# Kernel optimization log

Measured on AMD Instinct MI355X. Metric: run time of the kernel, lower is better.

The kernel has to match this reference:

```python
import jax, jax.numpy as jnp
import numpy as np

N_NODES = 50000
N_EDGES = 800000
N_FEAT = 32
DIM_ENC = 64
HEADS = 8
DIM_MLP = 512
NUM_GRAPHS = 2000
NEG_SLOPE = 0.2


def gat_conv(x, edge_index, W, a_src, a_dst, bias, concat):
    """PyG-style GATConv: add self loops, per-head attention, segment softmax over
    incoming edges at the destination node, weighted scatter-sum aggregation."""
    N = x.shape[0]
    H, F = a_src.shape
    h = (x @ W).reshape(N, H, F)                      # [N, H, F]
    loop = jnp.arange(N, dtype=edge_index.dtype)
    src = jnp.concatenate([edge_index[0], loop])      # source j
    dst = jnp.concatenate([edge_index[1], loop])      # target i
    alpha_src = (h * a_src[None]).sum(-1)             # [N, H]
    alpha_dst = (h * a_dst[None]).sum(-1)             # [N, H]
    e = alpha_src[src] + alpha_dst[dst]               # [E', H]
    e = jnp.where(e > 0, e, NEG_SLOPE * e)            # leaky_relu
    # segment softmax over edges sharing the same destination node
    m = jax.ops.segment_max(e, dst, num_segments=N)
    ex = jnp.exp(e - m[dst])
    s = jax.ops.segment_sum(ex, dst, num_segments=N)
    alpha = ex / (s[dst] + 1e-16)                     # [E', H]
    msg = h[src] * alpha[..., None]                   # [E', H, F]
    out = jax.ops.segment_sum(msg, dst, num_segments=N)  # [N, H, F]
    out = out.reshape(N, H * F) if concat else out.mean(axis=1)
    return out + bias


def setup_inputs() -> dict:
    key = jax.random.key(0)
    ks = jax.random.split(key, 16)
    x = jax.random.normal(ks[0], (N_NODES, N_FEAT), dtype=jnp.float32)
    edge_index = jax.random.randint(ks[1], (2, N_EDGES), 0, N_NODES, dtype=jnp.int64)
    batch = jnp.sort(jax.random.randint(ks[2], (N_NODES,), 0, NUM_GRAPHS, dtype=jnp.int64))
    sc = lambda fi, fo: 1.0 / np.sqrt(fi)
    W1 = jax.random.normal(ks[3], (N_FEAT, HEADS * DIM_ENC), dtype=jnp.float32) * sc(N_FEAT, 0)
    a_src1 = jax.random.normal(ks[4], (HEADS, DIM_ENC), dtype=jnp.float32) * sc(DIM_ENC, 0)
    a_dst1 = jax.random.normal(ks[5], (HEADS, DIM_ENC), dtype=jnp.float32) * sc(DIM_ENC, 0)
    b1 = jnp.zeros((DIM_ENC,), dtype=jnp.float32)
    W2 = jax.random.normal(ks[6], (DIM_ENC, HEADS * DIM_ENC), dtype=jnp.float32) * sc(DIM_ENC, 0)
    a_src2 = jax.random.normal(ks[7], (HEADS, DIM_ENC), dtype=jnp.float32) * sc(DIM_ENC, 0)
    a_dst2 = jax.random.normal(ks[8], (HEADS, DIM_ENC), dtype=jnp.float32) * sc(DIM_ENC, 0)
    b2 = jnp.zeros((HEADS * DIM_ENC,), dtype=jnp.float32)
    fcW1 = jax.random.normal(ks[9], (HEADS * DIM_ENC, DIM_MLP), dtype=jnp.float32) * sc(HEADS * DIM_ENC, 0)
    fcb1 = jnp.zeros((DIM_MLP,), dtype=jnp.float32)
    fcW2 = jax.random.normal(ks[10], (DIM_MLP, DIM_MLP), dtype=jnp.float32) * sc(DIM_MLP, 0)
    fcb2 = jnp.zeros((DIM_MLP,), dtype=jnp.float32)
    fcW3 = jax.random.normal(ks[11], (DIM_MLP, 1), dtype=jnp.float32) * sc(DIM_MLP, 0)
    fcb3 = jnp.zeros((1,), dtype=jnp.float32)
    return dict(x=x, edge_index=edge_index, batch=batch,
                W1=W1, a_src1=a_src1, a_dst1=a_dst1, b1=b1,
                W2=W2, a_src2=a_src2, a_dst2=a_dst2, b2=b2,
                fcW1=fcW1, fcb1=fcb1, fcW2=fcW2, fcb2=fcb2, fcW3=fcW3, fcb3=fcb3)


def reference(x, edge_index, batch, W1, a_src1, a_dst1, b1, W2, a_src2, a_dst2, b2,
              fcW1, fcb1, fcW2, fcb2, fcW3, fcb3):
    h = gat_conv(x, edge_index, W1, a_src1, a_dst1, b1, concat=False)   # [N, dim_enc]
    h = gat_conv(h, edge_index, W2, a_src2, a_dst2, b2, concat=True)    # [N, 8*dim_enc]
    g = jax.ops.segment_sum(h, batch, num_segments=NUM_GRAPHS)          # [G, 8*dim_enc]
    g = jax.nn.relu(g @ fcW1 + fcb1)   # dropout is identity in eval / p=0
    g = jax.nn.relu(g @ fcW2 + fcb2)
    return g @ fcW3 + fcb3             # [G, 1]
```

## Files before the change

### kernel.cpp

```cpp
#include <hip/hip_runtime.h>
#include <hip/hip_bf16.h>

#define N_NODES   50000
#define N_EDGES   800000
#define NF        32
#define DE        64
#define NH        8
#define CT        512
#define DMLP      512
#define NG        2000
#define NEGS      0.2f


__device__ inline float4 fma4(float a, float4 v, float4 c) {
    c.x = fmaf(a, v.x, c.x); c.y = fmaf(a, v.y, c.y);
    c.z = fmaf(a, v.z, c.z); c.w = fmaf(a, v.w, c.w);
    return c;
}

__device__ inline float edge_w(float e) {
    e = e > 0.f ? e : NEGS * e;
    return __expf(e);
}


#define SB_A 1563
#define SB_I 196
#define SB_U 64
#define SB_G 196
#define SB_B 2

__global__ __launch_bounds__(256) void setup_k(
        const float* __restrict__ x, const float* __restrict__ W1,
        const float* __restrict__ as1, const float* __restrict__ ad1,
        const float* __restrict__ W2, const float* __restrict__ as2,
        const float* __restrict__ ad2, const int* __restrict__ batch,
        int* __restrict__ cnt, int* __restrict__ cur, int* __restrict__ total,
        float* __restrict__ U1, int* __restrict__ goff,
        float* __restrict__ B2s, float* __restrict__ B2d,
        float* __restrict__ as_, float* __restrict__ ad_) {
    int b = blockIdx.x;
    int tid = threadIdx.x;
    if (b < SB_A) {
        __shared__ float bs[256], bd[256];
        {
            int c = tid >> 3, hd = tid & 7;
            const float* wr = W1 + c * 512 + hd * 64;
            const float* p1 = as1 + hd * 64;
            const float* p2 = ad1 + hd * 64;
            float s1 = 0.f, s2 = 0.f;
            #pragma unroll 8
            for (int f = 0; f < 64; ++f) { float w = wr[f]; s1 += w * p1[f]; s2 += w * p2[f]; }
            bs[tid] = s1; bd[tid] = s2;
        }
        __syncthreads();
        int gid = b * 256 + tid;
        if (gid < N_NODES * NH) {
            int n = gid >> 3, hd = gid & 7;
            const float4* xp = (const float4*)(x + (size_t)n * NF);
            float s1 = 0.f, s2 = 0.f;
            #pragma unroll
            for (int qq = 0; qq < NF / 4; ++qq) {
                float4 v = xp[qq];
                int b0 = qq * 32 + hd;
                s1 += v.x * bs[b0] + v.y * bs[b0 + 8] + v.z * bs[b0 + 16] + v.w * bs[b0 + 24];
                s2 += v.x * bd[b0] + v.y * bd[b0 + 8] + v.z * bd[b0 + 16] + v.w * bd[b0 + 24];
            }
            as_[gid] = s1;
            ad_[gid] = s2;
        }
    } else if (b < SB_A + SB_I) {
        int i = (b - SB_A) * 256 + tid;
        if (i < N_NODES) { cnt[i] = 1; cur[i] = 0; }
        if (i == 0) total[0] = 0;
    } else if (b < SB_A + SB_I + SB_U) {
        int i = (b - SB_A - SB_I) * 256 + tid;
        int k = i >> 6, f = i & 63;
        int hd = k >> 5, c = k & 31;
        U1[i] = W1[c * 512 + hd * 64 + f] * 0.125f;
    } else if (b < SB_A + SB_I + SB_U + SB_G) {
        int i = (b - SB_A - SB_I - SB_U) * 256 + tid;
        if (i < N_NODES) {
            int bb = batch[i];
            if (i == 0) {
                for (int g = 0; g <= bb; ++g) goff[g] = 0;
            } else {
                int pb = batch[i - 1];
                for (int g = pb + 1; g <= bb; ++g) goff[g] = i;
            }
            if (i == N_NODES - 1) {
                for (int g = bb + 1; g <= NG; ++g) goff[g] = N_NODES;
            }
        }
    } else {
        int i = (b - SB_A - SB_I - SB_U - SB_G) * 256 + tid;
        int c = i >> 3, hd = i & 7;
        const float* wr = W2 + c * 512 + hd * 64;
        const float* p1 = as2 + hd * 64;
        const float* p2 = ad2 + hd * 64;
        float s1 = 0.f, s2 = 0.f;
        #pragma unroll 8
        for (int f = 0; f < 64; ++f) { float w = wr[f]; s1 += w * p1[f]; s2 += w * p2[f]; }
        B2s[i] = s1; B2d[i] = s2;
    }
}


__global__ void hist_k(const int* __restrict__ ei, int* __restrict__ cnt) {
    int e = blockIdx.x * 256 + threadIdx.x;
    if (e < N_EDGES) atomicAdd(&cnt[ei[N_EDGES + e]], 1);
}

__global__ void alloc_off_k(const int* __restrict__ cnt, int* __restrict__ off,
                            int* __restrict__ total) {
    int i = blockIdx.x * 256 + threadIdx.x;
    if (i < N_NODES) off[i] = atomicAdd(total, cnt[i]);
}

__global__ void scatter_k(const int* __restrict__ ei, const int* __restrict__ off,
                          int* __restrict__ cur, int* __restrict__ ssrc) {
    int e = blockIdx.x * 256 + threadIdx.x;
    if (e < N_EDGES) {
        int s = ei[e];
        int d = ei[N_EDGES + e];
        int p = off[d] + atomicAdd(&cur[d], 1);
        ssrc[p] = s;
    } else if (e < N_EDGES + N_NODES) {
        int i = e - N_EDGES;
        int p = off[i] + atomicAdd(&cur[i], 1);
        ssrc[p] = i;
    }
}


__global__ void alpha2_k(const float* __restrict__ hx, const float* __restrict__ Bs,
                         const float* __restrict__ Bd, float* __restrict__ as_,
                         float* __restrict__ ad_) {
    __shared__ float bs[512], bd[512];
    int tid = threadIdx.x;
    for (int i = tid; i < 512; i += 256) { bs[i] = Bs[i]; bd[i] = Bd[i]; }
    __syncthreads();
    int gid = blockIdx.x * 256 + tid;
    if (gid >= N_NODES * NH) return;
    int n = gid >> 3, hd = gid & 7;
    const float4* xp = (const float4*)(hx + (size_t)n * DE);
    float s1 = 0.f, s2 = 0.f;
    #pragma unroll
    for (int qq = 0; qq < DE / 4; ++qq) {
        float4 v = xp[qq];
        int b0 = qq * 32 + hd;
        s1 += v.x * bs[b0] + v.y * bs[b0 + 8] + v.z * bs[b0 + 16] + v.w * bs[b0 + 24];
        s2 += v.x * bd[b0] + v.y * bd[b0 + 8] + v.z * bd[b0 + 16] + v.w * bd[b0 + 24];
    }
    as_[gid] = s1;
    ad_[gid] = s2;
}


__global__ __launch_bounds__(256) void agg1_k(
        const float* __restrict__ x, const float* __restrict__ as_,
        const float* __restrict__ ad_, const int* __restrict__ ssrc,
        const int* __restrict__ off, const int* __restrict__ cnt,
        float* __restrict__ aggx1) {
    int wv = __builtin_amdgcn_readfirstlane(blockIdx.x * 4 + (threadIdx.x >> 6));
    if (wv >= N_NODES) return;
    int lane = threadIdx.x & 63;
    int hd = lane >> 3, q = lane & 7;
    int beg = off[wv], end = beg + cnt[wv];
    float adv = ad_[wv * NH + hd];

    float4 acc = {0.f, 0.f, 0.f, 0.f};
    float wsum = 0.f;
    int j = beg;
    for (; j + 8 <= end; j += 8) {
        int s[8]; float ev[8]; float4 v[8];
        #pragma unroll
        for (int u = 0; u < 8; ++u) s[u] = ssrc[j + u];
        #pragma unroll
        for (int u = 0; u < 8; ++u) ev[u] = as_[s[u] * NH + hd];
        #pragma unroll
        for (int u = 0; u < 8; ++u) v[u] = *(const float4*)(x + s[u] * NF + q * 4);
        #pragma unroll
        for (int u = 0; u < 8; ++u) {
            float w = edge_w(ev[u] + adv);
            wsum += w;
            acc = fma4(w, v[u], acc);
        }
    }
    for (; j < end; ++j) {
        int s0 = ssrc[j];
        float w0 = edge_w(as_[s0 * NH + hd] + adv);
        float4 v0 = *(const float4*)(x + s0 * NF + q * 4);
        wsum += w0;
        acc = fma4(w0, v0, acc);
    }
    float inv = 1.f / wsum;
    acc.x *= inv; acc.y *= inv; acc.z *= inv; acc.w *= inv;
    ((float4*)(aggx1 + (size_t)wv * 256))[lane] = acc;
}


template<int K, int N, bool RELU>
__global__ __launch_bounds__(256) void tgemm_k(
        const float* __restrict__ A, const float* __restrict__ W,
        const float* __restrict__ bias, float* __restrict__ Y, int nrows) {
    constexpr int KC = (K < 256) ? K : 256;
    __shared__ float As[KC][64];
    int t = threadIdx.x;
    int row0 = blockIdx.x * 64;
    int col0 = blockIdx.y * 64;
    int rr = t & 63;
    int kb = (t >> 6) * (KC / 4);
    int r0 = (t >> 4) * 4;
    int c0 = (t & 15) * 4;
    float acc[4][4];
    #pragma unroll
    for (int i = 0; i < 4; ++i)
        #pragma unroll
        for (int j = 0; j < 4; ++j) acc[i][j] = 0.f;

    for (int kc = 0; kc < K; kc += KC) {
        if (kc) __syncthreads();
        {
            int grow = row0 + rr;
            const float* ap = A + (size_t)grow * K + kc + kb;
            #pragma unroll
            for (int i = 0; i < KC / 4; i += 4) {
                float4 v = {0.f, 0.f, 0.f, 0.f};
                if (grow < nrows) v = *(const float4*)(ap + i);
                As[kb + i + 0][rr] = v.x;
                As[kb + i + 1][rr] = v.y;
                As[kb + i + 2][rr] = v.z;
                As[kb + i + 3][rr] = v.w;
            }
        }
        __syncthreads();
        const float* wp = W + (size_t)kc * N + col0 + c0;
        #pragma unroll 4
        for (int k = 0; k < KC; ++k) {
            float4 a = *(const float4*)&As[k][r0];
            float4 w = *(const float4*)(wp + (size_t)k * N);
            acc[0][0] = fmaf(a.x, w.x, acc[0][0]); acc[0][1] = fmaf(a.x, w.y, acc[0][1]);
            acc[0][2] = fmaf(a.x, w.z, acc[0][2]); acc[0][3] = fmaf(a.x, w.w, acc[0][3]);
            acc[1][0] = fmaf(a.y, w.x, acc[1][0]); acc[1][1] = fmaf(a.y, w.y, acc[1][1]);
            acc[1][2] = fmaf(a.y, w.z, acc[1][2]); acc[1][3] = fmaf(a.y, w.w, acc[1][3]);
            acc[2][0] = fmaf(a.z, w.x, acc[2][0]); acc[2][1] = fmaf(a.z, w.y, acc[2][1]);
            acc[2][2] = fmaf(a.z, w.z, acc[2][2]); acc[2][3] = fmaf(a.z, w.w, acc[2][3]);
            acc[3][0] = fmaf(a.w, w.x, acc[3][0]); acc[3][1] = fmaf(a.w, w.y, acc[3][1]);
            acc[3][2] = fmaf(a.w, w.z, acc[3][2]); acc[3][3] = fmaf(a.w, w.w, acc[3][3]);
        }
    }
    float4 bv = *(const float4*)(bias + col0 + c0);
    #pragma unroll
    for (int i = 0; i < 4; ++i) {
        int row = row0 + r0 + i;
        if (row < nrows) {
            float4 o;
            o.x = acc[i][0] + bv.x; o.y = acc[i][1] + bv.y;
            o.z = acc[i][2] + bv.z; o.w = acc[i][3] + bv.w;
            if (RELU) {
                o.x = fmaxf(o.x, 0.f); o.y = fmaxf(o.y, 0.f);
                o.z = fmaxf(o.z, 0.f); o.w = fmaxf(o.w, 0.f);
            }
            *(float4*)&Y[(size_t)row * N + col0 + c0] = o;
        }
    }
}


__global__ __launch_bounds__(512) void agg2gp_k(
        const float* __restrict__ hx, const float* __restrict__ as_,
        const float* __restrict__ ad_, const int* __restrict__ ssrc,
        const int* __restrict__ off, const int* __restrict__ cnt,
        const int* __restrict__ goff, const float* __restrict__ W2,
        const float* __restrict__ b2, float* __restrict__ g0) {
    int g = blockIdx.x;
    int w = threadIdx.x >> 6;
    int lane = threadIdx.x & 63;
    int hd = lane >> 3, q = lane & 7;
    int nbeg = goff[g], nend = goff[g + 1];

    __shared__ float sp[8][512];
    __shared__ float ps[512];

    float4 p0 = {0.f, 0.f, 0.f, 0.f}, p1 = {0.f, 0.f, 0.f, 0.f};

    for (int nd0 = nbeg + w; nd0 < nend; nd0 += 8) {
        int nd = __builtin_amdgcn_readfirstlane(nd0);
        int beg = off[nd], end = beg + cnt[nd];
        float adv = ad_[nd * NH + hd];

        float4 a0 = {0.f, 0.f, 0.f, 0.f}, a1 = {0.f, 0.f, 0.f, 0.f};
        float wsum = 0.f;
        int j = beg;
        for (; j + 4 <= end; j += 4) {
            int s0 = ssrc[j], s1 = ssrc[j + 1], s2 = ssrc[j + 2], s3 = ssrc[j + 3];
            float e0 = as_[s0 * NH + hd], e1 = as_[s1 * NH + hd];
            float e2 = as_[s2 * NH + hd], e3 = as_[s3 * NH + hd];
            const float4* pp0 = (const float4*)(hx + s0 * DE + q * 8);
            const float4* pp1 = (const float4*)(hx + s1 * DE + q * 8);
            const float4* pp2 = (const float4*)(hx + s2 * DE + q * 8);
            const float4* pp3 = (const float4*)(hx + s3 * DE + q * 8);
            float4 v00 = pp0[0], v01 = pp0[1];
            float4 v10 = pp1[0], v11 = pp1[1];
            float4 v20 = pp2[0], v21 = pp2[1];
            float4 v30 = pp3[0], v31 = pp3[1];
            float w0 = edge_w(e0 + adv), w1 = edge_w(e1 + adv);
            float w2 = edge_w(e2 + adv), w3 = edge_w(e3 + adv);
            wsum += (w0 + w1) + (w2 + w3);
            a0 = fma4(w0, v00, a0); a1 = fma4(w0, v01, a1);
            a0 = fma4(w1, v10, a0); a1 = fma4(w1, v11, a1);
            a0 = fma4(w2, v20, a0); a1 = fma4(w2, v21, a1);
            a0 = fma4(w3, v30, a0); a1 = fma4(w3, v31, a1);
        }
        for (; j < end; ++j) {
            int s0 = ssrc[j];
            float w0 = edge_w(as_[s0 * NH + hd] + adv);
            const float4* pp0 = (const float4*)(hx + s0 * DE + q * 8);
            float4 v00 = pp0[0], v01 = pp0[1];
            wsum += w0;
            a0 = fma4(w0, v00, a0); a1 = fma4(w0, v01, a1);
        }
        float inv = 1.f / wsum;
        p0 = fma4(inv, a0, p0);
        p1 = fma4(inv, a1, p1);
    }

    *(float4*)&sp[w][lane * 8]     = p0;
    *(float4*)&sp[w][lane * 8 + 4] = p1;
    __syncthreads();
    int t = threadIdx.x;
    {
        float s = 0.f;
        #pragma unroll
        for (int ww = 0; ww < 8; ++ww) s += sp[ww][t];
        ps[t] = s;
    }
    __syncthreads();

    int hd2 = t >> 6, f = t & 63;
    int cn = nend - nbeg;
    float acc = (float)cn * b2[t];
    const float* pp = &ps[hd2 * 64];
    const float* wp = W2 + hd2 * 64 + f;
    #pragma unroll 8
    for (int c = 0; c < 64; ++c)
        acc = fmaf(pp[c], wp[(size_t)c * 512], acc);
    g0[(size_t)g * CT + t] = acc;
}


__global__ void mlp_out_k(const float* __restrict__ gin, const float* __restrict__ w,
                          const float* __restrict__ b, float* __restrict__ out) {
    int row = blockIdx.x * 4 + (threadIdx.x >> 6);
    int lane = threadIdx.x & 63;
    if (row >= NG) return;
    float s = 0.f;
    for (int k = lane; k < DMLP; k += 64) s += gin[(size_t)row * DMLP + k] * w[k];
    #pragma unroll
    for (int d = 32; d >= 1; d >>= 1) s += __shfl_xor(s, d, 64);
    if (lane == 0) out[row] = s + b[0];
}


extern "C" void kernel_launch(void* const* d_in, const int* in_sizes, int n_in,
                              void* d_out, int out_size, void* d_ws, size_t ws_size,
                              hipStream_t stream) {
    const float* x     = (const float*)d_in[0];
    const int*   ei    = (const int*)d_in[1];
    const int*   batch = (const int*)d_in[2];
    const float* W1    = (const float*)d_in[3];
    const float* asrc1 = (const float*)d_in[4];
    const float* adst1 = (const float*)d_in[5];
    const float* b1    = (const float*)d_in[6];
    const float* W2    = (const float*)d_in[7];
    const float* asrc2 = (const float*)d_in[8];
    const float* adst2 = (const float*)d_in[9];
    const float* b2    = (const float*)d_in[10];
    const float* fcW1  = (const float*)d_in[11];
    const float* fcb1  = (const float*)d_in[12];
    const float* fcW2  = (const float*)d_in[13];
    const float* fcb2  = (const float*)d_in[14];
    const float* fcW3  = (const float*)d_in[15];
    const float* fcb3  = (const float*)d_in[16];

    char* p = (char*)d_ws;
    auto take = [&](size_t bytes) {
        char* r = p;
        p += (bytes + 255) & ~(size_t)255;
        return r;
    };
    float* aggx1 = (float*)take((size_t)N_NODES * 256 * 4);
    float* hx    = (float*)take((size_t)N_NODES * DE * 4);
    float* as_   = (float*)take((size_t)N_NODES * NH * 4);
    float* ad_   = (float*)take((size_t)N_NODES * NH * 4);
    int*   ssrc  = (int*)take((size_t)(N_EDGES + N_NODES) * 4);
    int*   offv  = (int*)take((size_t)N_NODES * 4);
    int*   cntv  = (int*)take((size_t)N_NODES * 4);
    int*   cur   = (int*)take((size_t)N_NODES * 4);
    int*   total = (int*)take(256);
    int*   goff  = (int*)take((size_t)(NG + 1) * 4);
    float* B2s   = (float*)take(512 * 4);
    float* B2d   = (float*)take(512 * 4);
    float* U1    = (float*)take(256 * 64 * 4);
    float* g0    = (float*)take((size_t)NG * DMLP * 4);
    float* g1    = (float*)take((size_t)NG * DMLP * 4);
    float* g2    = (float*)take((size_t)NG * DMLP * 4);

    setup_k<<<SB_A + SB_I + SB_U + SB_G + SB_B, 256, 0, stream>>>(
        x, W1, asrc1, adst1, W2, asrc2, adst2, batch,
        cntv, cur, total, U1, goff, B2s, B2d, as_, ad_);

    hist_k<<<(N_EDGES + 255) / 256, 256, 0, stream>>>(ei, cntv);
    alloc_off_k<<<(N_NODES + 255) / 256, 256, 0, stream>>>(cntv, offv, total);
    scatter_k<<<(N_EDGES + N_NODES + 255) / 256, 256, 0, stream>>>(ei, offv, cur, ssrc);

    agg1_k<<<(N_NODES + 3) / 4, 256, 0, stream>>>(x, as_, ad_, ssrc, offv, cntv, aggx1);
    {
        dim3 grid((N_NODES + 63) / 64, 1);
        tgemm_k<256, 64, false><<<grid, 256, 0, stream>>>(aggx1, U1, b1, hx, N_NODES);
    }

    alpha2_k<<<(N_NODES * NH + 255) / 256, 256, 0, stream>>>(hx, B2s, B2d, as_, ad_);
    agg2gp_k<<<NG, 512, 0, stream>>>(hx, as_, ad_, ssrc, offv, cntv, goff, W2, b2, g0);

    {
        dim3 grid((NG + 63) / 64, DMLP / 64);
        tgemm_k<DMLP, DMLP, true><<<grid, 256, 0, stream>>>(g0, fcW1, fcb1, g1, NG);
        tgemm_k<DMLP, DMLP, true><<<grid, 256, 0, stream>>>(g1, fcW2, fcb2, g2, NG);
    }
    mlp_out_k<<<(NG + 3) / 4, 256, 0, stream>>>(g2, fcW3, fcb3, (float*)d_out);
}
```

Measured before the change: 426.6 us.

## Fuse alpha2 into layer-1 projection and final MLP dot into last GEMM

Folds the layer-2 attention coefficient computation into the layer-1 projection GEMM epilogue, so hx is not re-read by a separate kernel. Fuses the final 512->1 dot product into the second MLP GEMM using shared-memory partial sums and atomicAdd into an output pre-initialised with the bias in setup. Also shrinks the agg2gp block to 4 waves, reduces agg1 unroll from 8 to 4, and uses 64-wide K chunks in the GEMMs. Adds kernel-count reduction at the cost of atomics and a non-deterministic summation order in the output.

```diff
diff --git a/kernel.cpp b/kernel.cpp
--- a/kernel.cpp
+++ b/kernel.cpp
@@ -29,16 +29,19 @@
 #define SB_U 64
 #define SB_G 196
 #define SB_B 2
+#define SB_O 8
 
 __global__ __launch_bounds__(256) void setup_k(
         const float* __restrict__ x, const float* __restrict__ W1,
         const float* __restrict__ as1, const float* __restrict__ ad1,
         const float* __restrict__ W2, const float* __restrict__ as2,
         const float* __restrict__ ad2, const int* __restrict__ batch,
+        const float* __restrict__ fcb3,
         int* __restrict__ cnt, int* __restrict__ cur, int* __restrict__ total,
         float* __restrict__ U1, int* __restrict__ goff,
         float* __restrict__ B2s, float* __restrict__ B2d,
-        float* __restrict__ as_, float* __restrict__ ad_) {
+        float* __restrict__ as_, float* __restrict__ ad_,
+        float* __restrict__ outp) {
     int b = blockIdx.x;
     int tid = threadIdx.x;
     if (b < SB_A) {
@@ -92,7 +95,7 @@
                 for (int g = bb + 1; g <= NG; ++g) goff[g] = N_NODES;
             }
         }
-    } else {
+    } else if (b < SB_A + SB_I + SB_U + SB_G + SB_B) {
         int i = (b - SB_A - SB_I - SB_U - SB_G) * 256 + tid;
         int c = i >> 3, hd = i & 7;
         const float* wr = W2 + c * 512 + hd * 64;
@@ -102,6 +105,9 @@
         #pragma unroll 8
         for (int f = 0; f < 64; ++f) { float w = wr[f]; s1 += w * p1[f]; s2 += w * p2[f]; }
         B2s[i] = s1; B2d[i] = s2;
+    } else {
+        int i = (b - SB_A - SB_I - SB_U - SB_G - SB_B) * 256 + tid;
+        if (i < NG) outp[i] = fcb3[0];
     }
 }
 
@@ -133,30 +139,6 @@
 }
 
 
-__global__ void alpha2_k(const float* __restrict__ hx, const float* __restrict__ Bs,
-                         const float* __restrict__ Bd, float* __restrict__ as_,
-                         float* __restrict__ ad_) {
-    __shared__ float bs[512], bd[512];
-    int tid = threadIdx.x;
-    for (int i = tid; i < 512; i += 256) { bs[i] = Bs[i]; bd[i] = Bd[i]; }
-    __syncthreads();
-    int gid = blockIdx.x * 256 + tid;
-    if (gid >= N_NODES * NH) return;
-    int n = gid >> 3, hd = gid & 7;
-    const float4* xp = (const float4*)(hx + (size_t)n * DE);
-    float s1 = 0.f, s2 = 0.f;
-    #pragma unroll
-    for (int qq = 0; qq < DE / 4; ++qq) {
-        float4 v = xp[qq];
-        int b0 = qq * 32 + hd;
-        s1 += v.x * bs[b0] + v.y * bs[b0 + 8] + v.z * bs[b0 + 16] + v.w * bs[b0 + 24];
-        s2 += v.x * bd[b0] + v.y * bd[b0 + 8] + v.z * bd[b0 + 16] + v.w * bd[b0 + 24];
-    }
-    as_[gid] = s1;
-    ad_[gid] = s2;
-}
-
-
 __global__ __launch_bounds__(256) void agg1_k(
         const float* __restrict__ x, const float* __restrict__ as_,
         const float* __restrict__ ad_, const int* __restrict__ ssrc,
@@ -172,20 +154,19 @@
     float4 acc = {0.f, 0.f, 0.f, 0.f};
     float wsum = 0.f;
     int j = beg;
-    for (; j + 8 <= end; j += 8) {
-        int s[8]; float ev[8]; float4 v[8];
-        #pragma unroll
-        for (int u = 0; u < 8; ++u) s[u] = ssrc[j + u];
-        #pragma unroll
-        for (int u = 0; u < 8; ++u) ev[u] = as_[s[u] * NH + hd];
-        #pragma unroll
-        for (int u = 0; u < 8; ++u) v[u] = *(const float4*)(x + s[u] * NF + q * 4);
-        #pragma unroll
-        for (int u = 0; u < 8; ++u) {
-            float w = edge_w(ev[u] + adv);
-            wsum += w;
-            acc = fma4(w, v[u], acc);
-        }
+    for (; j + 4 <= end; j += 4) {
+        int s0 = ssrc[j], s1 = ssrc[j + 1], s2 = ssrc[j + 2], s3 = ssrc[j + 3];
+        float e0 = as_[s0 * NH + hd], e1 = as_[s1 * NH + hd];
+        float e2 = as_[s2 * NH + hd], e3 = as_[s3 * NH + hd];
+        float4 v0 = *(const float4*)(x + s0 * NF + q * 4);
+        float4 v1 = *(const float4*)(x + s1 * NF + q * 4);
+        float4 v2 = *(const float4*)(x + s2 * NF + q * 4);
+        float4 v3 = *(const float4*)(x + s3 * NF + q * 4);
+        float w0 = edge_w(e0 + adv), w1 = edge_w(e1 + adv);
+        float w2 = edge_w(e2 + adv), w3 = edge_w(e3 + adv);
+        wsum += (w0 + w1) + (w2 + w3);
+        acc = fma4(w0, v0, acc); acc = fma4(w1, v1, acc);
+        acc = fma4(w2, v2, acc); acc = fma4(w3, v3, acc);
     }
     for (; j < end; ++j) {
         int s0 = ssrc[j];
@@ -200,17 +181,18 @@
 }
 
 
-template<int K, int N, bool RELU>
-__global__ __launch_bounds__(256) void tgemm_k(
-        const float* __restrict__ A, const float* __restrict__ W,
-        const float* __restrict__ bias, float* __restrict__ Y, int nrows) {
-    constexpr int KC = (K < 256) ? K : 256;
-    __shared__ float As[KC][64];
+__global__ __launch_bounds__(256) void proj1a_k(
+        const float* __restrict__ A, const float* __restrict__ U1,
+        const float* __restrict__ b1, const float* __restrict__ B2s,
+        const float* __restrict__ B2d, float* __restrict__ hx,
+        float* __restrict__ as_, float* __restrict__ ad_) {
+    __shared__ float As[64][64];
+    __shared__ float bs2[512], bd2[512];
     int t = threadIdx.x;
     int row0 = blockIdx.x * 64;
-    int col0 = blockIdx.y * 64;
+    for (int i = t; i < 512; i += 256) { bs2[i] = B2s[i]; bd2[i] = B2d[i]; }
     int rr = t & 63;
-    int kb = (t >> 6) * (KC / 4);
+    int kb = (t >> 6) * 16;
     int r0 = (t >> 4) * 4;
     int c0 = (t & 15) * 4;
     float acc[4][4];
@@ -219,15 +201,15 @@
         #pragma unroll
         for (int j = 0; j < 4; ++j) acc[i][j] = 0.f;
 
-    for (int kc = 0; kc < K; kc += KC) {
-        if (kc) __syncthreads();
+    for (int kc = 0; kc < 256; kc += 64) {
+        __syncthreads();
         {
             int grow = row0 + rr;
-            const float* ap = A + (size_t)grow * K + kc + kb;
+            const float* ap = A + (size_t)grow * 256 + kc + kb;
             #pragma unroll
-            for (int i = 0; i < KC / 4; i += 4) {
+            for (int i = 0; i < 16; i += 4) {
                 float4 v = {0.f, 0.f, 0.f, 0.f};
-                if (grow < nrows) v = *(const float4*)(ap + i);
+                if (grow < N_NODES) v = *(const float4*)(ap + i);
                 As[kb + i + 0][rr] = v.x;
                 As[kb + i + 1][rr] = v.y;
                 As[kb + i + 2][rr] = v.z;
@@ -235,11 +217,11 @@
             }
         }
         __syncthreads();
-        const float* wp = W + (size_t)kc * N + col0 + c0;
+        const float* wp = U1 + (size_t)kc * 64 + c0;
         #pragma unroll 4
-        for (int k = 0; k < KC; ++k) {
+        for (int k = 0; k < 64; ++k) {
             float4 a = *(const float4*)&As[k][r0];
-            float4 w = *(const float4*)(wp + (size_t)k * N);
+            float4 w = *(const float4*)(wp + k * 64);
             acc[0][0] = fmaf(a.x, w.x, acc[0][0]); acc[0][1] = fmaf(a.x, w.y, acc[0][1]);
             acc[0][2] = fmaf(a.x, w.z, acc[0][2]); acc[0][3] = fmaf(a.x, w.w, acc[0][3]);
             acc[1][0] = fmaf(a.y, w.x, acc[1][0]); acc[1][1] = fmaf(a.y, w.y, acc[1][1]);
@@ -250,25 +232,56 @@
             acc[3][2] = fmaf(a.w, w.z, acc[3][2]); acc[3][3] = fmaf(a.w, w.w, acc[3][3]);
         }
     }
-    float4 bv = *(const float4*)(bias + col0 + c0);
+    __syncthreads();
+    float4 bv = *(const float4*)(b1 + c0);
     #pragma unroll
     for (int i = 0; i < 4; ++i) {
-        int row = row0 + r0 + i;
-        if (row < nrows) {
-            float4 o;
-            o.x = acc[i][0] + bv.x; o.y = acc[i][1] + bv.y;
-            o.z = acc[i][2] + bv.z; o.w = acc[i][3] + bv.w;
-            if (RELU) {
-                o.x = fmaxf(o.x, 0.f); o.y = fmaxf(o.y, 0.f);
-                o.z = fmaxf(o.z, 0.f); o.w = fmaxf(o.w, 0.f);
-            }
-            *(float4*)&Y[(size_t)row * N + col0 + c0] = o;
-        }
-    }
-}
-
-
-__global__ __launch_bounds__(512) void agg2gp_k(
+        As[r0 + i][c0 + 0] = acc[i][0] + bv.x;
+        As[r0 + i][c0 + 1] = acc[i][1] + bv.y;
+        As[r0 + i][c0 + 2] = acc[i][2] + bv.z;
+        As[r0 + i][c0 + 3] = acc[i][3] + bv.w;
+    }
+    __syncthreads();
+    int row = t >> 2, sub = t & 3;
+    int grow = row0 + row;
+    float ps[8], pd[8];
+    #pragma unroll
+    for (int hd = 0; hd < 8; ++hd) { ps[hd] = 0.f; pd[hd] = 0.f; }
+    #pragma unroll 4
+    for (int c2 = 0; c2 < 16; ++c2) {
+        int c = sub * 16 + c2;
+        float v = As[row][c];
+        #pragma unroll
+        for (int hd = 0; hd < 8; ++hd) {
+            ps[hd] = fmaf(v, bs2[c * 8 + hd], ps[hd]);
+            pd[hd] = fmaf(v, bd2[c * 8 + hd], pd[hd]);
+        }
+    }
+    #pragma unroll
+    for (int d = 1; d <= 2; d <<= 1) {
+        #pragma unroll
+        for (int hd = 0; hd < 8; ++hd) {
+            ps[hd] += __shfl_xor(ps[hd], d, 64);
+            pd[hd] += __shfl_xor(pd[hd], d, 64);
+        }
+    }
+    if (grow < N_NODES) {
+        int h0 = sub * 2;
+        as_[grow * 8 + h0]     = ps[h0];
+        as_[grow * 8 + h0 + 1] = ps[h0 + 1];
+        ad_[grow * 8 + h0]     = pd[h0];
+        ad_[grow * 8 + h0 + 1] = pd[h0 + 1];
+        const float* r = &As[row][sub * 16];
+        float* dst = hx + (size_t)grow * 64 + sub * 16;
+        *(float4*)(dst + 0)  = *(const float4*)(r + 0);
+        *(float4*)(dst + 4)  = *(const float4*)(r + 4);
+        *(float4*)(dst + 8)  = *(const float4*)(r + 8);
+        *(float4*)(dst + 12) = *(const float4*)(r + 12);
+    }
+}
+
+
+__global__ __launch_bounds__(256) void agg2gp_k(
         const float* __restrict__ hx, const float* __restrict__ as_,
         const float* __restrict__ ad_, const int* __restrict__ ssrc,
         const int* __restrict__ off, const int* __restrict__ cnt,
@@ -280,12 +293,11 @@
     int hd = lane >> 3, q = lane & 7;
     int nbeg = goff[g], nend = goff[g + 1];
 
-    __shared__ float sp[8][512];
-    __shared__ float ps[512];
+    __shared__ float sp[4][512];
 
     float4 p0 = {0.f, 0.f, 0.f, 0.f}, p1 = {0.f, 0.f, 0.f, 0.f};
 
-    for (int nd0 = nbeg + w; nd0 < nend; nd0 += 8) {
+    for (int nd0 = nbeg + w; nd0 < nend; nd0 += 4) {
         int nd = __builtin_amdgcn_readfirstlane(nd0);
         int beg = off[nd], end = beg + cnt[nd];
         float adv = ad_[nd * NH + hd];
@@ -297,10 +309,10 @@
             int s0 = ssrc[j], s1 = ssrc[j + 1], s2 = ssrc[j + 2], s3 = ssrc[j + 3];
             float e0 = as_[s0 * NH + hd], e1 = as_[s1 * NH + hd];
             float e2 = as_[s2 * NH + hd], e3 = as_[s3 * NH + hd];
-            const float4* pp0 = (const float4*)(hx + s0 * DE + q * 8);
-            const float4* pp1 = (const float4*)(hx + s1 * DE + q * 8);
-            const float4* pp2 = (const float4*)(hx + s2 * DE + q * 8);
-            const float4* pp3 = (const float4*)(hx + s3 * DE + q * 8);
+            const float4* pp0 = (const float4*)(hx + (size_t)s0 * DE + q * 8);
+            const float4* pp1 = (const float4*)(hx + (size_t)s1 * DE + q * 8);
+            const float4* pp2 = (const float4*)(hx + (size_t)s2 * DE + q * 8);
+            const float4* pp3 = (const float4*)(hx + (size_t)s3 * DE + q * 8);
             float4 v00 = pp0[0], v01 = pp0[1];
             float4 v10 = pp1[0], v11 = pp1[1];
             float4 v20 = pp2[0], v21 = pp2[1];
@@ -316,7 +328,7 @@
         for (; j < end; ++j) {
             int s0 = ssrc[j];
             float w0 = edge_w(as_[s0 * NH + hd] + adv);
-            const float4* pp0 = (const float4*)(hx + s0 * DE + q * 8);
+            const float4* pp0 = (const float4*)(hx + (size_t)s0 * DE + q * 8);
             float4 v00 = pp0[0], v01 = pp0[1];
             wsum += w0;
             a0 = fma4(w0, v00, a0); a1 = fma4(w0, v01, a1);
@@ -331,35 +343,113 @@
     __syncthreads();
     int t = threadIdx.x;
     {
-        float s = 0.f;
+        float s0 = sp[0][t] + sp[1][t] + sp[2][t] + sp[3][t];
+        float s1 = sp[0][t + 256] + sp[1][t + 256] + sp[2][t + 256] + sp[3][t + 256];
+        sp[0][t] = s0;
+        sp[0][t + 256] = s1;
+    }
+    __syncthreads();
+    int cn = nend - nbeg;
+    #pragma unroll
+    for (int half = 0; half < 2; ++half) {
+        int ch = t + half * 256;
+        int hd2 = ch >> 6;
+        float acc = (float)cn * b2[ch];
+        const float* pp = &sp[0][hd2 * 64];
+        #pragma unroll 8
+        for (int c = 0; c < 64; ++c)
+            acc = fmaf(pp[c], W2[(size_t)c * 512 + ch], acc);
+        g0[(size_t)g * CT + ch] = acc;
+    }
+}
+
+
+template<bool RELU, bool FINAL>
+__global__ __launch_bounds__(256) void tgemm_k(
+        const float* __restrict__ A, const float* __restrict__ W,
+        const float* __restrict__ bias, float* __restrict__ Y, int nrows,
+        const float* __restrict__ W3, float* __restrict__ outp) {
+    constexpr int K = 512, N = 512;
+    __shared__ float As[64][64];
+    int t = threadIdx.x;
+    int row0 = blockIdx.x * 64;
+    int col0 = blockIdx.y * 64;
+    int rr = t & 63;
+    int kb = (t >> 6) * 16;
+    int r0 = (t >> 4) * 4;
+    int c0 = (t & 15) * 4;
+    float acc[4][4];
+    #pragma unroll
+    for (int i = 0; i < 4; ++i)
         #pragma unroll
-        for (int ww = 0; ww < 8; ++ww) s += sp[ww][t];
-        ps[t] = s;
-    }
-    __syncthreads();
-
-    int hd2 = t >> 6, f = t & 63;
-    int cn = nend - nbeg;
-    float acc = (float)cn * b2[t];
-    const float* pp = &ps[hd2 * 64];
-    const float* wp = W2 + hd2 * 64 + f;
-    #pragma unroll 8
-    for (int c = 0; c < 64; ++c)
-        acc = fmaf(pp[c], wp[(size_t)c * 512], acc);
-    g0[(size_t)g * CT + t] = acc;
-}
-
-
-__global__ void mlp_out_k(const float* __restrict__ gin, const float* __restrict__ w,
-                          const float* __restrict__ b, float* __restrict__ out) {
-    int row = blockIdx.x * 4 + (threadIdx.x >> 6);
-    int lane = threadIdx.x & 63;
-    if (row >= NG) return;
-    float s = 0.f;
-    for (int k = lane; k < DMLP; k += 64) s += gin[(size_t)row * DMLP + k] * w[k];
-    #pragma unroll
-    for (int d = 32; d >= 1; d >>= 1) s += __shfl_xor(s, d, 64);
-    if (lane == 0) out[row] = s + b[0];
+        for (int j = 0; j < 4; ++j) acc[i][j] = 0.f;
+
+    for (int kc = 0; kc < K; kc += 64) {
+        __syncthreads();
+        {
+            int grow = row0 + rr;
+            const float* ap = A + (size_t)grow * K + kc + kb;
+            #pragma unroll
+            for (int i = 0; i < 16; i += 4) {
+                float4 v = {0.f, 0.f, 0.f, 0.f};
+                if (grow < nrows) v = *(const float4*)(ap + i);
+                As[kb + i + 0][rr] = v.x;
+                As[kb + i + 1][rr] = v.y;
+                As[kb + i + 2][rr] = v.z;
+                As[kb + i + 3][rr] = v.w;
+            }
+        }
+        __syncthreads();
+        const float* wp = W + (size_t)kc * N + col0 + c0;
+        #pragma unroll 4
+        for (int k = 0; k < 64; ++k) {
+            float4 a = *(const float4*)&As[k][r0];
+            float4 w = *(const float4*)(wp + (size_t)k * N);
+            acc[0][0] = fmaf(a.x, w.x, acc[0][0]); acc[0][1] = fmaf(a.x, w.y, acc[0][1]);
+            acc[0][2] = fmaf(a.x, w.z, acc[0][2]); acc[0][3] = fmaf(a.x, w.w, acc[0][3]);
+            acc[1][0] = fmaf(a.y, w.x, acc[1][0]); acc[1][1] = fmaf(a.y, w.y, acc[1][1]);
+            acc[1][2] = fmaf(a.y, w.z, acc[1][2]); acc[1][3] = fmaf(a.y, w.w, acc[1][3]);
+            acc[2][0] = fmaf(a.z, w.x, acc[2][0]); acc[2][1] = fmaf(a.z, w.y, acc[2][1]);
+            acc[2][2] = fmaf(a.z, w.z, acc[2][2]); acc[2][3] = fmaf(a.z, w.w, acc[2][3]);
+            acc[3][0] = fmaf(a.w, w.x, acc[3][0]); acc[3][1] = fmaf(a.w, w.y, acc[3][1]);
+            acc[3][2] = fmaf(a.w, w.z, acc[3][2]); acc[3][3] = fmaf(a.w, w.w, acc[3][3]);
+        }
+    }
+    float4 bv = *(const float4*)(bias + col0 + c0);
+    if constexpr (!FINAL) {
+        #pragma unroll
+        for (int i = 0; i < 4; ++i) {
+            int row = row0 + r0 + i;
+            if (row < nrows) {
+                float4 o;
+                o.x = acc[i][0] + bv.x; o.y = acc[i][1] + bv.y;
+                o.z = acc[i][2] + bv.z; o.w = acc[i][3] + bv.w;
+                if (RELU) {
+                    o.x = fmaxf(o.x, 0.f); o.y = fmaxf(o.y, 0.f);
+                    o.z = fmaxf(o.z, 0.f); o.w = fmaxf(o.w, 0.f);
+                }
+                *(float4*)&Y[(size_t)row * N + col0 + c0] = o;
+            }
+        }
+    } else {
+        __shared__ float ps2[64][17];
+        float4 w3 = *(const float4*)(W3 + col0 + c0);
+        #pragma unroll
+        for (int i = 0; i < 4; ++i) {
+            float4 o;
+            o.x = fmaxf(acc[i][0] + bv.x, 0.f); o.y = fmaxf(acc[i][1] + bv.y, 0.f);
+            o.z = fmaxf(acc[i][2] + bv.z, 0.f); o.w = fmaxf(acc[i][3] + bv.w, 0.f);
+            ps2[r0 + i][t & 15] = o.x * w3.x + o.y * w3.y + o.z * w3.z + o.w * w3.w;
+        }
+        __syncthreads();
+        if (t < 64) {
+            float s = 0.f;
+            #pragma unroll
+            for (int jj = 0; jj < 16; ++jj) s += ps2[t][jj];
+            int row = row0 + t;
+            if (row < nrows) atomicAdd(&outp[row], s);
+        }
+    }
 }
 
 
@@ -383,6 +473,7 @@
     const float* fcb2  = (const float*)d_in[14];
     const float* fcW3  = (const float*)d_in[15];
     const float* fcb3  = (const float*)d_in[16];
+    float* outp = (float*)d_out;
 
     char* p = (char*)d_ws;
     auto take = [&](size_t bytes) {
@@ -405,29 +496,23 @@
     float* U1    = (float*)take(256 * 64 * 4);
     float* g0    = (float*)take((size_t)NG * DMLP * 4);
     float* g1    = (float*)take((size_t)NG * DMLP * 4);
-    float* g2    = (float*)take((size_t)NG * DMLP * 4);
-
-    setup_k<<<SB_A + SB_I + SB_U + SB_G + SB_B, 256, 0, stream>>>(
-        x, W1, asrc1, adst1, W2, asrc2, adst2, batch,
-        cntv, cur, total, U1, goff, B2s, B2d, as_, ad_);
+
+    setup_k<<<SB_A + SB_I + SB_U + SB_G + SB_B + SB_O, 256, 0, stream>>>(
+        x, W1, asrc1, adst1, W2, asrc2, adst2, batch, fcb3,
+        cntv, cur, total, U1, goff, B2s, B2d, as_, ad_, outp);
 
     hist_k<<<(N_EDGES + 255) / 256, 256, 0, stream>>>(ei, cntv);
     alloc_off_k<<<(N_NODES + 255) / 256, 256, 0, stream>>>(cntv, offv, total);
     scatter_k<<<(N_EDGES + N_NODES + 255) / 256, 256, 0, stream>>>(ei, offv, cur, ssrc);
 
     agg1_k<<<(N_NODES + 3) / 4, 256, 0, stream>>>(x, as_, ad_, ssrc, offv, cntv, aggx1);
-    {
-        dim3 grid((N_NODES + 63) / 64, 1);
-        tgemm_k<256, 64, false><<<grid, 256, 0, stream>>>(aggx1, U1, b1, hx, N_NODES);
-    }
-
-    alpha2_k<<<(N_NODES * NH + 255) / 256, 256, 0, stream>>>(hx, B2s, B2d, as_, ad_);
-    agg2gp_k<<<NG, 512, 0, stream>>>(hx, as_, ad_, ssrc, offv, cntv, goff, W2, b2, g0);
+    proj1a_k<<<(N_NODES + 63) / 64, 256, 0, stream>>>(aggx1, U1, b1, B2s, B2d, hx, as_, ad_);
+
+    agg2gp_k<<<NG, 256, 0, stream>>>(hx, as_, ad_, ssrc, offv, cntv, goff, W2, b2, g0);
 
     {
         dim3 grid((NG + 63) / 64, DMLP / 64);
-        tgemm_k<DMLP, DMLP, true><<<grid, 256, 0, stream>>>(g0, fcW1, fcb1, g1, NG);
-        tgemm_k<DMLP, DMLP, true><<<grid, 256, 0, stream>>>(g1, fcW2, fcb2, g2, NG);
-    }
-    mlp_out_k<<<(NG + 3) / 4, 256, 0, stream>>>(g2, fcW3, fcb3, (float*)d_out);
-}
+        tgemm_k<true, false><<<grid, 256, 0, stream>>>(g0, fcW1, fcb1, g1, NG, nullptr, nullptr);
+        tgemm_k<true, true><<<grid, 256, 0, stream>>>(g1, fcW2, fcb2, nullptr, NG, fcW3, outp);
+    }
+}
```

New measurement: 409.1 us. 4.1% less time.
